# Kernel tuning notes

Hardware: AMD Instinct MI355X
Metric: run time of the kernel (lower is better)

## Reference

```python
import jax, jax.numpy as jnp
import numpy as np

B, S, D, V = 16384, 20, 128, 12  # batch, max_seq_len, embed_dim, num_embeddings
EPS = 1e-5


def _rmsnorm_ax1(x, w):
    # RMSNorm over axis=1 of [B, S, D], learnable scale of shape [S]
    ms = jnp.mean(x * x, axis=1, keepdims=True)
    return x * jax.lax.rsqrt(ms + EPS) * w[None, :, None]


def _dwconv(x, w, b, dil):
    # depthwise conv1d: x [B, S, D], w [S, 1, K], groups=S, 'same' padding
    y = jax.lax.conv_general_dilated(
        x, w, window_strides=(1,), padding=[(dil, dil)],
        rhs_dilation=(dil,), dimension_numbers=('NCH', 'OIH', 'NCH'),
        feature_group_count=x.shape[1])
    return y + b[None, :, None]


def setup_inputs() -> dict:
    key = jax.random.key(0)
    ks = jax.random.split(key, 14)
    sc = 0.05
    return {
        'tokens': jax.random.randint(ks[0], (B, S), 0, V, dtype=jnp.int32),
        'number_log': jax.random.normal(ks[1], (B,), dtype=jnp.float32),
        'emb': jax.random.normal(ks[2], (V, D), dtype=jnp.float32) * sc,
        'pre_w': jnp.ones((S,), dtype=jnp.float32),
        'w0': jax.random.normal(ks[3], (S, 1, 3), dtype=jnp.float32) * sc,
        'b0': jax.random.normal(ks[4], (S,), dtype=jnp.float32) * sc,
        'w1': jax.random.normal(ks[5], (S, 1, 3), dtype=jnp.float32) * sc,
        'b1': jax.random.normal(ks[6], (S,), dtype=jnp.float32) * sc,
        'w2': jax.random.normal(ks[7], (S, 1, 3), dtype=jnp.float32) * sc,
        'b2': jax.random.normal(ks[8], (S,), dtype=jnp.float32) * sc,
        'gate_w': jax.random.normal(ks[9], (S, S), dtype=jnp.float32) * sc,
        'gate_b': jax.random.normal(ks[10], (S,), dtype=jnp.float32) * sc,
        'post_w': jnp.ones((S,), dtype=jnp.float32),
        'logit_w': jax.random.normal(ks[11], (1, S, 1), dtype=jnp.float32) * sc,
    }


def reference(tokens, number_log, emb, pre_w, w0, b0, w1, b1, w2, b2,
              gate_w, gate_b, post_w, logit_w):
    x = emb[tokens]                       # [B, S, D] embedding lookup
    x_norm = _rmsnorm_ax1(x, pre_w)       # pre RMSNorm over seq axis
    x_d = (_dwconv(x_norm, w0, b0, 1)
           + _dwconv(x_norm, w1, b1, 2)
           + _dwconv(x_norm, w2, b2, 4))  # multi-dilation depthwise branches
    # gate: Linear(S,S)+SiLU applied along axis 1 (torch transposes to [B,D,S])
    g = jnp.einsum('bsl,ts->btl', x_norm, gate_w) + gate_b[None, :, None]
    g = jax.nn.silu(g)
    x_d = _rmsnorm_ax1(x_d * g, post_w)
    # final pointwise conv1d S->1, no bias
    out = jnp.einsum('bsl,os->bol', x + x_d, logit_w[:, :, 0])  # [B, 1, D]
    return out
```

## Files before the change

kernel.cpp:

```cpp
#include <hip/hip_runtime.h>
#include <stdint.h>

#define BB 16384
#define SS 20
#define DD 128
#define EPSV 1e-5f


typedef __fp16 half2_t __attribute__((ext_vector_type(2)));

#define BPERMU(addr, v) ((uint32_t)__builtin_amdgcn_ds_bpermute((addr), (int)(v)))

static __device__ __forceinline__ uint32_t pk16(float a, float b) {
    return __builtin_bit_cast(uint32_t, __builtin_amdgcn_cvt_pkrtz(a, b));
}
static __device__ __forceinline__ half2_t h2(uint32_t u) {
    return __builtin_bit_cast(half2_t, u);
}

__global__ void pack_w_kernel(const float* __restrict__ gate_w,
                              const float* __restrict__ w0, const float* __restrict__ b0,
                              const float* __restrict__ w1, const float* __restrict__ b1,
                              const float* __restrict__ w2, const float* __restrict__ b2,
                              uint32_t*    __restrict__ ws) {
    const int i = threadIdx.x;
    if (i < SS * SS) {
        const float v = gate_w[i];
        ws[i] = pk16(v, v);
    }
    if (i < SS) {
        const float wa0 = w0[i*3+0], wam = w0[i*3+1], wa2 = w0[i*3+2];
        const float wb0 = w1[i*3+0], wbm = w1[i*3+1], wb2 = w1[i*3+2];
        const float wc0 = w2[i*3+0], wcm = w2[i*3+1], wc2 = w2[i*3+2];
        const float cw   = wam + wbm + wcm;
        const float bias = b0[i] + b1[i] + b2[i];
        uint32_t* o = ws + SS * SS + i * 8;
        o[0] = pk16(wc0, wc0);  o[1] = pk16(wb0, wb0);
        o[2] = pk16(wa0, wa0);  o[3] = pk16(cw,  cw);
        o[4] = pk16(wa2, wa2);  o[5] = pk16(wb2, wb2);
        o[6] = pk16(wc2, wc2);  o[7] = pk16(bias, bias);
    }
}

__global__ __launch_bounds__(256) void fused_mdt_kernel(
    const int*      __restrict__ tokens,
    const float*    __restrict__ emb,
    const float*    __restrict__ pre_w,
    const uint32_t* __restrict__ wpk,
    const float*    __restrict__ gate_b,
    const float*    __restrict__ post_w,
    const float*    __restrict__ logit_w,
    float*          __restrict__ out)
{
    const int tid  = threadIdx.x;
    const int lane = tid & 63;
    const int il   = lane & 31;
    const int b    = blockIdx.x * 8 + (tid >> 5);
    const int d0   = il << 2;

    const bool mL = (il == 0);
    const bool mR = (il == 31);
    const int  la = (lane - 1) << 2;
    const int  ra = (lane + 1) << 2;

    const int4* t4 = reinterpret_cast<const int4*>(tokens + b * SS);

    float ms0=0.f, ms1=0.f, ms2=0.f, ms3=0.f;
    float a10=0.f, a11=0.f, a12=0.f, a13=0.f;
    #pragma unroll
    for (int i = 0; i < 5; ++i) {
        const int4 tv = t4[i];
        const int tg[4] = {tv.x, tv.y, tv.z, tv.w};
        #pragma unroll
        for (int j = 0; j < 4; ++j) {
            const int s = 4*i + j;
            const float4 v = *reinterpret_cast<const float4*>(emb + tg[j] * DD + d0);
            ms0 = fmaf(v.x, v.x, ms0); ms1 = fmaf(v.y, v.y, ms1);
            ms2 = fmaf(v.z, v.z, ms2); ms3 = fmaf(v.w, v.w, ms3);
            const float lw = logit_w[s];
            a10 = fmaf(v.x, lw, a10); a11 = fmaf(v.y, lw, a11);
            a12 = fmaf(v.z, lw, a12); a13 = fmaf(v.w, lw, a13);
        }
    }
    const float r0 = rsqrtf(ms0 * (1.f/SS) + EPSV);
    const float r1 = rsqrtf(ms1 * (1.f/SS) + EPSV);
    const float r2 = rsqrtf(ms2 * (1.f/SS) + EPSV);
    const float r3 = rsqrtf(ms3 * (1.f/SS) + EPSV);

    __builtin_amdgcn_sched_barrier(0);

    uint32_t X0[SS], X1[SS];
    #pragma unroll
    for (int i = 0; i < 5; ++i) {
        const int4 tv = t4[i];
        const int tg[4] = {tv.x, tv.y, tv.z, tv.w};
        #pragma unroll
        for (int j = 0; j < 4; ++j) {
            const int s = 4*i + j;
            const float4 v = *reinterpret_cast<const float4*>(emb + tg[j] * DD + d0);
            const float pw = pre_w[s];
            X0[s] = pk16(v.x * (r0 * pw), v.y * (r1 * pw));
            X1[s] = pk16(v.z * (r2 * pw), v.w * (r3 * pw));
        }
    }

    __builtin_amdgcn_sched_barrier(0);

    float m20=0.f, m21=0.f, m22=0.f, m23=0.f;
    float ac0=0.f, ac1=0.f, ac2=0.f, ac3=0.f;
    #pragma unroll
    for (int t = 0; t < SS; ++t) {
        uint32_t LX0 = BPERMU(la, X0[t]);
        uint32_t LX1 = BPERMU(la, X1[t]);
        uint32_t RX0 = BPERMU(ra, X0[t]);
        uint32_t RX1 = BPERMU(ra, X1[t]);
        LX0 = mL ? 0u : LX0;  LX1 = mL ? 0u : LX1;
        RX0 = mR ? 0u : RX0;  RX1 = mR ? 0u : RX1;
        const uint32_t Dm1 = __builtin_amdgcn_alignbit(X0[t], LX1, 16);
        const uint32_t Dc  = __builtin_amdgcn_alignbit(X1[t], X0[t], 16);
        const uint32_t Dp1 = __builtin_amdgcn_alignbit(RX0, X1[t], 16);

        const uint32_t* cw8 = wpk + SS * SS + t * 8;
        half2_t xdA = h2(cw8[7]);
        xdA += h2(cw8[0]) * h2(LX0);
        xdA += h2(cw8[1]) * h2(LX1);
        xdA += h2(cw8[2]) * h2(Dm1);
        xdA += h2(cw8[3]) * h2(X0[t]);
        xdA += h2(cw8[4]) * h2(Dc);
        xdA += h2(cw8[5]) * h2(X1[t]);
        xdA += h2(cw8[6]) * h2(RX0);
        half2_t xdB = h2(cw8[7]);
        xdB += h2(cw8[0]) * h2(LX1);
        xdB += h2(cw8[1]) * h2(X0[t]);
        xdB += h2(cw8[2]) * h2(Dc);
        xdB += h2(cw8[3]) * h2(X1[t]);
        xdB += h2(cw8[4]) * h2(Dp1);
        xdB += h2(cw8[5]) * h2(RX0);
        xdB += h2(cw8[6]) * h2(RX1);

        half2_t gaA = h2(0u), gbA = h2(0u), gaB = h2(0u), gbB = h2(0u);
        #pragma unroll
        for (int q = 0; q < SS / 2; ++q) {
            const half2_t hw0 = h2(wpk[t * SS + 2*q    ]);
            const half2_t hw1 = h2(wpk[t * SS + 2*q + 1]);
            gaA += hw0 * h2(X0[2*q    ]);
            gbA += hw1 * h2(X0[2*q + 1]);
            gaB += hw0 * h2(X1[2*q    ]);
            gbB += hw1 * h2(X1[2*q + 1]);
        }
        const half2_t gpA = gaA + gbA;
        const half2_t gpB = gaB + gbB;
        const float gbv = gate_b[t];
        const float g0 = (float)gpA[0] + gbv;
        const float g1 = (float)gpA[1] + gbv;
        const float g2 = (float)gpB[0] + gbv;
        const float g3 = (float)gpB[1] + gbv;
        const float xd0 = (float)xdA[0], xd1 = (float)xdA[1];
        const float xd2 = (float)xdB[0], xd3 = (float)xdB[1];

        const float pl = post_w[t] * logit_w[t];
        const float h0 = xd0 * (g0 * __builtin_amdgcn_rcpf(1.f + __expf(-g0)));
        const float h1 = xd1 * (g1 * __builtin_amdgcn_rcpf(1.f + __expf(-g1)));
        const float h2v = xd2 * (g2 * __builtin_amdgcn_rcpf(1.f + __expf(-g2)));
        const float h3 = xd3 * (g3 * __builtin_amdgcn_rcpf(1.f + __expf(-g3)));
        m20 = fmaf(h0, h0, m20); m21 = fmaf(h1, h1, m21);
        m22 = fmaf(h2v, h2v, m22); m23 = fmaf(h3, h3, m23);
        ac0 = fmaf(h0, pl, ac0); ac1 = fmaf(h1, pl, ac1);
        ac2 = fmaf(h2v, pl, ac2); ac3 = fmaf(h3, pl, ac3);
    }

    const float q0 = rsqrtf(m20 * (1.f/SS) + EPSV);
    const float q1 = rsqrtf(m21 * (1.f/SS) + EPSV);
    const float q2 = rsqrtf(m22 * (1.f/SS) + EPSV);
    const float q3 = rsqrtf(m23 * (1.f/SS) + EPSV);

    float4 res;
    res.x = a10 + q0 * ac0;
    res.y = a11 + q1 * ac1;
    res.z = a12 + q2 * ac2;
    res.w = a13 + q3 * ac3;
    *reinterpret_cast<float4*>(out + b * DD + d0) = res;
}

extern "C" void kernel_launch(void* const* d_in, const int* in_sizes, int n_in,
                              void* d_out, int out_size, void* d_ws, size_t ws_size,
                              hipStream_t stream) {
    const int*   tokens  = (const int*)  d_in[0];
    const float* emb     = (const float*)d_in[2];
    const float* pre_w   = (const float*)d_in[3];
    const float* w0      = (const float*)d_in[4];
    const float* b0      = (const float*)d_in[5];
    const float* w1      = (const float*)d_in[6];
    const float* b1      = (const float*)d_in[7];
    const float* w2      = (const float*)d_in[8];
    const float* b2      = (const float*)d_in[9];
    const float* gate_w  = (const float*)d_in[10];
    const float* gate_b  = (const float*)d_in[11];
    const float* post_w  = (const float*)d_in[12];
    const float* logit_w = (const float*)d_in[13];
    float*       out     = (float*)d_out;
    uint32_t*    ws      = (uint32_t*)d_ws;

    hipLaunchKernelGGL(pack_w_kernel, dim3(1), dim3(512), 0, stream,
                       gate_w, w0, b0, w1, b1, w2, b2, ws);

    dim3 grid(BB / 8);
    dim3 block(256);
    hipLaunchKernelGGL(fused_mdt_kernel, grid, block, 0, stream,
                       tokens, emb, pre_w, (const uint32_t*)ws,
                       gate_b, post_w, logit_w, out);
}
```

Before: 52.09 us.

## Move SiLU, RMSNorm accumulation and residual path to packed fp16

Converts the gate SiLU, post-RMSNorm sum-of-squares, logit accumulation and residual logit dot product from fp32 scalar math to packed half2 operations. Gate bias, post*logit and logit weights are pre-packed into a widened 16-word per-row record. The second embedding gather is removed by keeping the raw packed values and rescaling them in place. This halves ALU work and memory re-reads, but fp16 accumulation of squared sums and the residual can lose precision or overflow.

Result: faster. 47.32 us (-9.2%).

```diff
diff --git a/kernel.cpp b/kernel.cpp
--- a/kernel.cpp
+++ b/kernel.cpp
@@ -1,4 +1,5 @@
 #include <hip/hip_runtime.h>
+#include <hip/hip_fp16.h>
 #include <stdint.h>
 
 #define BB 16384
@@ -7,21 +8,25 @@
 #define EPSV 1e-5f
 
 
-typedef __fp16 half2_t __attribute__((ext_vector_type(2)));
-
 #define BPERMU(addr, v) ((uint32_t)__builtin_amdgcn_ds_bpermute((addr), (int)(v)))
 
 static __device__ __forceinline__ uint32_t pk16(float a, float b) {
     return __builtin_bit_cast(uint32_t, __builtin_amdgcn_cvt_pkrtz(a, b));
 }
-static __device__ __forceinline__ half2_t h2(uint32_t u) {
-    return __builtin_bit_cast(half2_t, u);
+static __device__ __forceinline__ __half2 H2(uint32_t u) {
+    return __builtin_bit_cast(__half2, u);
+}
+static __device__ __forceinline__ uint32_t U32(__half2 h) {
+    return __builtin_bit_cast(uint32_t, h);
 }
 
 __global__ void pack_w_kernel(const float* __restrict__ gate_w,
                               const float* __restrict__ w0, const float* __restrict__ b0,
                               const float* __restrict__ w1, const float* __restrict__ b1,
                               const float* __restrict__ w2, const float* __restrict__ b2,
+                              const float* __restrict__ gate_b,
+                              const float* __restrict__ post_w,
+                              const float* __restrict__ logit_w,
                               uint32_t*    __restrict__ ws) {
     const int i = threadIdx.x;
     if (i < SS * SS) {
@@ -34,11 +39,17 @@
         const float wc0 = w2[i*3+0], wcm = w2[i*3+1], wc2 = w2[i*3+2];
         const float cw   = wam + wbm + wcm;
         const float bias = b0[i] + b1[i] + b2[i];
-        uint32_t* o = ws + SS * SS + i * 8;
+        const float gbv  = gate_b[i];
+        const float pl   = post_w[i] * logit_w[i];
+        const float lw   = logit_w[i];
+        uint32_t* o = ws + SS * SS + i * 16;
         o[0] = pk16(wc0, wc0);  o[1] = pk16(wb0, wb0);
         o[2] = pk16(wa0, wa0);  o[3] = pk16(cw,  cw);
         o[4] = pk16(wa2, wa2);  o[5] = pk16(wb2, wb2);
         o[6] = pk16(wc2, wc2);  o[7] = pk16(bias, bias);
+        o[8] = pk16(gbv, gbv);  o[9] = pk16(pl, pl);
+        o[10] = pk16(lw, lw);
+        o[11] = 0u; o[12] = 0u; o[13] = 0u; o[14] = 0u; o[15] = 0u;
     }
 }
 
@@ -47,9 +58,6 @@
     const float*    __restrict__ emb,
     const float*    __restrict__ pre_w,
     const uint32_t* __restrict__ wpk,
-    const float*    __restrict__ gate_b,
-    const float*    __restrict__ post_w,
-    const float*    __restrict__ logit_w,
     float*          __restrict__ out)
 {
     const int tid  = threadIdx.x;
@@ -65,8 +73,9 @@
 
     const int4* t4 = reinterpret_cast<const int4*>(tokens + b * SS);
 
+    uint32_t X0[SS], X1[SS];
     float ms0=0.f, ms1=0.f, ms2=0.f, ms3=0.f;
-    float a10=0.f, a11=0.f, a12=0.f, a13=0.f;
+    __half2 a1pkA = H2(0u), a1pkB = H2(0u);
     #pragma unroll
     for (int i = 0; i < 5; ++i) {
         const int4 tv = t4[i];
@@ -77,9 +86,13 @@
             const float4 v = *reinterpret_cast<const float4*>(emb + tg[j] * DD + d0);
             ms0 = fmaf(v.x, v.x, ms0); ms1 = fmaf(v.y, v.y, ms1);
             ms2 = fmaf(v.z, v.z, ms2); ms3 = fmaf(v.w, v.w, ms3);
-            const float lw = logit_w[s];
-            a10 = fmaf(v.x, lw, a10); a11 = fmaf(v.y, lw, a11);
-            a12 = fmaf(v.z, lw, a12); a13 = fmaf(v.w, lw, a13);
+            const uint32_t xr0 = pk16(v.x, v.y);
+            const uint32_t xr1 = pk16(v.z, v.w);
+            const __half2 lwpk = H2(wpk[SS * SS + s * 16 + 10]);
+            a1pkA = __hfma2(H2(xr0), lwpk, a1pkA);
+            a1pkB = __hfma2(H2(xr1), lwpk, a1pkB);
+            X0[s] = xr0;
+            X1[s] = xr1;
         }
     }
     const float r0 = rsqrtf(ms0 * (1.f/SS) + EPSV);
@@ -87,27 +100,15 @@
     const float r2 = rsqrtf(ms2 * (1.f/SS) + EPSV);
     const float r3 = rsqrtf(ms3 * (1.f/SS) + EPSV);
 
-    __builtin_amdgcn_sched_barrier(0);
-
-    uint32_t X0[SS], X1[SS];
     #pragma unroll
-    for (int i = 0; i < 5; ++i) {
-        const int4 tv = t4[i];
-        const int tg[4] = {tv.x, tv.y, tv.z, tv.w};
-        #pragma unroll
-        for (int j = 0; j < 4; ++j) {
-            const int s = 4*i + j;
-            const float4 v = *reinterpret_cast<const float4*>(emb + tg[j] * DD + d0);
-            const float pw = pre_w[s];
-            X0[s] = pk16(v.x * (r0 * pw), v.y * (r1 * pw));
-            X1[s] = pk16(v.z * (r2 * pw), v.w * (r3 * pw));
-        }
-    }
-
-    __builtin_amdgcn_sched_barrier(0);
-
-    float m20=0.f, m21=0.f, m22=0.f, m23=0.f;
-    float ac0=0.f, ac1=0.f, ac2=0.f, ac3=0.f;
+    for (int s = 0; s < SS; ++s) {
+        const float pw = pre_w[s];
+        X0[s] = U32(__hmul2(H2(X0[s]), H2(pk16(r0 * pw, r1 * pw))));
+        X1[s] = U32(__hmul2(H2(X1[s]), H2(pk16(r2 * pw, r3 * pw))));
+    }
+
+    const __half2 one = __float2half2_rn(1.f);
+    __half2 m2pkA = H2(0u), m2pkB = H2(0u), acpkA = H2(0u), acpkB = H2(0u);
     #pragma unroll
     for (int t = 0; t < SS; ++t) {
         uint32_t LX0 = BPERMU(la, X0[t]);
@@ -120,65 +121,62 @@
         const uint32_t Dc  = __builtin_amdgcn_alignbit(X1[t], X0[t], 16);
         const uint32_t Dp1 = __builtin_amdgcn_alignbit(RX0, X1[t], 16);
 
-        const uint32_t* cw8 = wpk + SS * SS + t * 8;
-        half2_t xdA = h2(cw8[7]);
-        xdA += h2(cw8[0]) * h2(LX0);
-        xdA += h2(cw8[1]) * h2(LX1);
-        xdA += h2(cw8[2]) * h2(Dm1);
-        xdA += h2(cw8[3]) * h2(X0[t]);
-        xdA += h2(cw8[4]) * h2(Dc);
-        xdA += h2(cw8[5]) * h2(X1[t]);
-        xdA += h2(cw8[6]) * h2(RX0);
-        half2_t xdB = h2(cw8[7]);
-        xdB += h2(cw8[0]) * h2(LX1);
-        xdB += h2(cw8[1]) * h2(X0[t]);
-        xdB += h2(cw8[2]) * h2(Dc);
-        xdB += h2(cw8[3]) * h2(X1[t]);
-        xdB += h2(cw8[4]) * h2(Dp1);
-        xdB += h2(cw8[5]) * h2(RX0);
-        xdB += h2(cw8[6]) * h2(RX1);
-
-        half2_t gaA = h2(0u), gbA = h2(0u), gaB = h2(0u), gbB = h2(0u);
+        const uint32_t* rec = wpk + SS * SS + t * 16;
+        __half2 xdA = H2(rec[7]);
+        xdA = __hfma2(H2(rec[0]), H2(LX0),   xdA);
+        xdA = __hfma2(H2(rec[1]), H2(LX1),   xdA);
+        xdA = __hfma2(H2(rec[2]), H2(Dm1),   xdA);
+        xdA = __hfma2(H2(rec[3]), H2(X0[t]), xdA);
+        xdA = __hfma2(H2(rec[4]), H2(Dc),    xdA);
+        xdA = __hfma2(H2(rec[5]), H2(X1[t]), xdA);
+        xdA = __hfma2(H2(rec[6]), H2(RX0),   xdA);
+        __half2 xdB = H2(rec[7]);
+        xdB = __hfma2(H2(rec[0]), H2(LX1),   xdB);
+        xdB = __hfma2(H2(rec[1]), H2(X0[t]), xdB);
+        xdB = __hfma2(H2(rec[2]), H2(Dc),    xdB);
+        xdB = __hfma2(H2(rec[3]), H2(X1[t]), xdB);
+        xdB = __hfma2(H2(rec[4]), H2(Dp1),   xdB);
+        xdB = __hfma2(H2(rec[5]), H2(RX0),   xdB);
+        xdB = __hfma2(H2(rec[6]), H2(RX1),   xdB);
+
+        __half2 gaA = H2(rec[8]), gbA = H2(0u);
+        __half2 gaB = H2(rec[8]), gbB = H2(0u);
         #pragma unroll
         for (int q = 0; q < SS / 2; ++q) {
-            const half2_t hw0 = h2(wpk[t * SS + 2*q    ]);
-            const half2_t hw1 = h2(wpk[t * SS + 2*q + 1]);
-            gaA += hw0 * h2(X0[2*q    ]);
-            gbA += hw1 * h2(X0[2*q + 1]);
-            gaB += hw0 * h2(X1[2*q    ]);
-            gbB += hw1 * h2(X1[2*q + 1]);
+            const __half2 hw0 = H2(wpk[t * SS + 2*q    ]);
+            const __half2 hw1 = H2(wpk[t * SS + 2*q + 1]);
+            gaA = __hfma2(hw0, H2(X0[2*q    ]), gaA);
+            gbA = __hfma2(hw1, H2(X0[2*q + 1]), gbA);
+            gaB = __hfma2(hw0, H2(X1[2*q    ]), gaB);
+            gbB = __hfma2(hw1, H2(X1[2*q + 1]), gbB);
         }
-        const half2_t gpA = gaA + gbA;
-        const half2_t gpB = gaB + gbB;
-        const float gbv = gate_b[t];
-        const float g0 = (float)gpA[0] + gbv;
-        const float g1 = (float)gpA[1] + gbv;
-        const float g2 = (float)gpB[0] + gbv;
-        const float g3 = (float)gpB[1] + gbv;
-        const float xd0 = (float)xdA[0], xd1 = (float)xdA[1];
-        const float xd2 = (float)xdB[0], xd3 = (float)xdB[1];
-
-        const float pl = post_w[t] * logit_w[t];
-        const float h0 = xd0 * (g0 * __builtin_amdgcn_rcpf(1.f + __expf(-g0)));
-        const float h1 = xd1 * (g1 * __builtin_amdgcn_rcpf(1.f + __expf(-g1)));
-        const float h2v = xd2 * (g2 * __builtin_amdgcn_rcpf(1.f + __expf(-g2)));
-        const float h3 = xd3 * (g3 * __builtin_amdgcn_rcpf(1.f + __expf(-g3)));
-        m20 = fmaf(h0, h0, m20); m21 = fmaf(h1, h1, m21);
-        m22 = fmaf(h2v, h2v, m22); m23 = fmaf(h3, h3, m23);
-        ac0 = fmaf(h0, pl, ac0); ac1 = fmaf(h1, pl, ac1);
-        ac2 = fmaf(h2v, pl, ac2); ac3 = fmaf(h3, pl, ac3);
-    }
-
-    const float q0 = rsqrtf(m20 * (1.f/SS) + EPSV);
-    const float q1 = rsqrtf(m21 * (1.f/SS) + EPSV);
-    const float q2 = rsqrtf(m22 * (1.f/SS) + EPSV);
-    const float q3 = rsqrtf(m23 * (1.f/SS) + EPSV);
+        const __half2 gA = __hadd2(gaA, gbA);
+        const __half2 gB = __hadd2(gaB, gbB);
+
+        const __half2 eA  = h2exp(__hneg2(gA));
+        const __half2 eB  = h2exp(__hneg2(gB));
+        const __half2 rcA = h2rcp(__hadd2(one, eA));
+        const __half2 rcB = h2rcp(__hadd2(one, eB));
+        const __half2 hhA = __hmul2(xdA, __hmul2(gA, rcA));
+        const __half2 hhB = __hmul2(xdB, __hmul2(gB, rcB));
+
+        const __half2 plpk = H2(rec[9]);
+        m2pkA = __hfma2(hhA, hhA, m2pkA);
+        m2pkB = __hfma2(hhB, hhB, m2pkB);
+        acpkA = __hfma2(hhA, plpk, acpkA);
+        acpkB = __hfma2(hhB, plpk, acpkB);
+    }
+
+    const float q0 = rsqrtf(__low2float(m2pkA)  * (1.f/SS) + EPSV);
+    const float q1 = rsqrtf(__high2float(m2pkA) * (1.f/SS) + EPSV);
+    const float q2 = rsqrtf(__low2float(m2pkB)  * (1.f/SS) + EPSV);
+    const float q3 = rsqrtf(__high2float(m2pkB) * (1.f/SS) + EPSV);
 
     float4 res;
-    res.x = a10 + q0 * ac0;
-    res.y = a11 + q1 * ac1;
-    res.z = a12 + q2 * ac2;
-    res.w = a13 + q3 * ac3;
+    res.x = __low2float(a1pkA)  + q0 * __low2float(acpkA);
+    res.y = __high2float(a1pkA) + q1 * __high2float(acpkA);
+    res.z = __low2float(a1pkB)  + q2 * __low2float(acpkB);
+    res.w = __high2float(a1pkB) + q3 * __high2float(acpkB);
     *reinterpret_cast<float4*>(out + b * DD + d0) = res;
 }
 
@@ -202,11 +200,11 @@
     uint32_t*    ws      = (uint32_t*)d_ws;
 
     hipLaunchKernelGGL(pack_w_kernel, dim3(1), dim3(512), 0, stream,
-                       gate_w, w0, b0, w1, b1, w2, b2, ws);
+                       gate_w, w0, b0, w1, b1, w2, b2,
+                       gate_b, post_w, logit_w, ws);
 
     dim3 grid(BB / 8);
     dim3 block(256);
     hipLaunchKernelGGL(fused_mdt_kernel, grid, block, 0, stream,
-                       tokens, emb, pre_w, (const uint32_t*)ws,
-                       gate_b, post_w, logit_w, out);
-}
+                       tokens, emb, pre_w, (const uint32_t*)ws, out);
+}
```
